# Kernel tuning notes

Measured on AMD Instinct MI355X. Metric: run time of the kernel, lower is better.

The kernel has to match this reference:

```python
import jax, jax.numpy as jnp
import numpy as np
from functools import partial

ALPHA = 0.5
BETA = 0.5
THRESHOLD = 0.5


def _ccl(fg):
    """Connected-component labeling (4-connectivity) of a 2D bool mask via
    iterative min-label propagation; background = 0, components get distinct
    positive ids (component-wise min of raster index + 1). Matches the
    component partition of scipy.ndimage.label (ids differ, masks identical)."""
    H, W = fg.shape
    BIG = H * W + 2
    init = jnp.where(fg, jnp.arange(1, H * W + 1, dtype=jnp.int32).reshape(H, W), 0)

    def step(lab):
        l = jnp.where(fg, lab, BIG)
        up = jnp.pad(l, ((1, 0), (0, 0)), constant_values=BIG)[:-1]
        dn = jnp.pad(l, ((0, 1), (0, 0)), constant_values=BIG)[1:]
        lf = jnp.pad(l, ((0, 0), (1, 0)), constant_values=BIG)[:, :-1]
        rt = jnp.pad(l, ((0, 0), (0, 1)), constant_values=BIG)[:, 1:]
        m = jnp.minimum(jnp.minimum(jnp.minimum(up, dn), jnp.minimum(lf, rt)), l)
        return jnp.where(fg, m, 0)

    def cond(c):
        return jnp.any(c[0] != c[1])

    def body(c):
        return (step(c[0]), c[0])

    lab, _ = jax.lax.while_loop(cond, body, (step(init), init))
    return lab


def _critical(a_lab, b_lab, n_seg):
    """Binary mask of components of a_lab that are not fully covered by the
    foreground of b_lab (i.e. contain at least one mistake voxel) -- the
    detect_critical split/merge criterion."""
    miss = ((b_lab == 0) & (a_lab > 0)).astype(jnp.int32)
    counts = jax.ops.segment_sum(miss.ravel(), a_lab.ravel(), num_segments=n_seg)
    return jnp.where(a_lab > 0, (counts[a_lab] > 0).astype(jnp.float32), 0.0)


def _critical_masks(preds, targets):
    # preds/targets: [B,1,H,W]; work on channel-0 2D slices as the module does
    p2 = preds[:, 0]
    t2 = targets[:, 0]
    H, W = p2.shape[-2:]
    n_seg = H * W + 1
    plab = jax.vmap(_ccl)(p2 > THRESHOLD)
    tlab = jax.vmap(_ccl)(t2 > 0)
    crit = jax.vmap(partial(_critical, n_seg=n_seg))
    neg = crit(tlab, plab)   # critical_type = -1: target components missed
    pos = crit(plab, tlab)   # critical_type = +1: pred components wrong
    return BETA * neg + (1.0 - BETA) * pos  # [B,H,W]


def setup_inputs() -> dict:
    key = jax.random.key(0)
    k1, k2 = jax.random.split(key)
    preds = jax.random.normal(k1, (16, 1, 1024, 1024), dtype=jnp.float32)
    targets = (jax.random.uniform(k2, (16, 1, 1024, 1024)) > 0.5).astype(jnp.float32)
    return {"preds": preds, "targets": targets}


def reference(preds, targets):
    # BCEWithLogitsLoss(reduction='none'), numerically stable
    loss = jnp.maximum(preds, 0) - preds * targets + jnp.log1p(jnp.exp(-jnp.abs(preds)))
    mask = _critical_masks(preds, targets)  # [B,H,W], constant wrt grads
    weight = (1.0 - ALPHA) + ALPHA * mask[:, None]  # broadcast over channel dim
    return (weight * loss).mean()
```

## Files before the change

kernel.cpp:

```cpp
#include <hip/hip_runtime.h>
#include <math.h>


#define HH 1024
#define WW 1024
#define IMGPIX (HH * WW)
#define NB_TOTAL 16
#define FLAGBIT 0x40000000
#define IDXMASK 0x3FFFFFFF
#define NBLK 2048
#define NPART 2048
#define NTHR 256
#define WPR 16
#define RPR 512
#define SROWS 32
#define STRIPS (HH / SROWS)
#define SLOTS (SROWS * RPR)
#define NTHR_S 1024

typedef unsigned long long u64;

__device__ __forceinline__ int findRootH(int* p, int i) {
    volatile int* vp = p;
    int r = i;
    int e = vp[r] & IDXMASK;
    while (e != r) {
        int e2 = vp[e] & IDXMASK;
        if (e2 != e) p[r] = e2;
        r = e; e = e2;
    }
    return r;
}

__device__ __forceinline__ void flagProp(int* p, int x) {
    while (true) {
        int r = findRootH(p, x);
        int old = atomicOr(&p[r], FLAGBIT);
        if ((old & IDXMASK) == r) return;
        x = old & IDXMASK;
    }
}

__device__ __forceinline__ void uniteGF(int* p, int a, int b) {
    int ra = findRootH(p, a), rb = findRootH(p, b);
    while (ra != rb) {
        if (ra < rb) { int t = ra; ra = rb; rb = t; }
        int e = p[ra];
        if ((e & IDXMASK) != ra) { ra = findRootH(p, e & IDXMASK); continue; }
        int prev = atomicCAS(&p[ra], e, rb);
        if (prev == e) {
            if (e & FLAGBIT) flagProp(p, rb);
            return;
        }
        ra = findRootH(p, prev & IDXMASK);
        rb = findRootH(p, rb);
    }
}

__device__ __forceinline__ int findRootL(int* lab, int i) {
    volatile int* vl = lab;
    int r = i;
    int e = vl[r] & IDXMASK;
    while (e != r) {
        int e2 = vl[e] & IDXMASK;
        if (e2 != e) lab[r] = e2;
        r = e; e = e2;
    }
    return r;
}

__device__ __forceinline__ void uniteL(int* lab, int a, int b) {
    int ra = findRootL(lab, a), rb = findRootL(lab, b);
    while (ra != rb) {
        if (ra < rb) { int t = ra; ra = rb; rb = t; }
        int prev = atomicCAS(&lab[ra], ra, rb);
        if (prev == ra) return;
        ra = findRootL(lab, prev & IDXMASK);
        rb = findRootL(lab, rb);
    }
}

__device__ __forceinline__ int runIndexW(u64 starts, int b) {
    u64 below = (2ULL << b) - 1ULL;
    return (int)__popcll(starts & below) - 1;
}

__global__ void k_zero(double* __restrict__ part) {
    part[blockIdx.x * blockDim.x + threadIdx.x] = 0.0;
}

__global__ void k_maskloss(const float* __restrict__ preds, const float* __restrict__ targets,
                           long gbase, int nrows,
                           u64* __restrict__ fT, u64* __restrict__ fP,
                           u64* __restrict__ sT, u64* __restrict__ sP,
                           int* __restrict__ prT, int* __restrict__ prP,
                           int* __restrict__ rcT, int* __restrict__ rcP,
                           _Float16* __restrict__ lossH, double* __restrict__ part) {
    int wid = threadIdx.x >> 6, lane = threadIdx.x & 63;
    double lsum = 0.0;
    for (int R = blockIdx.x * 4 + wid; R < nrows; R += gridDim.x * 4) {
        long pixbase = (long)R * WW;
        u64 myW = 0;
        #pragma unroll 4
        for (int w = 0; w < WPR; ++w) {
            long g = gbase + pixbase + w * 64 + lane;
            float p = preds[g], t = targets[g];
            float loss = fmaxf(p, 0.0f) - p * t + __logf(1.0f + __expf(-fabsf(p)));
            lossH[pixbase + w * 64 + lane] = (_Float16)loss;
            lsum += (double)loss;
            u64 bt = __ballot(t > 0.0f);
            u64 bp = __ballot(p > 0.5f);
            if (lane == w) myW = bt;
            if (lane == w + 16) myW = bp;
        }
        if (lane < 32) {
            int subid = lane & 15;
            u64 prevW = __shfl_up(myW, 1, 16);
            u64 carry = (subid > 0) ? (prevW >> 63) : 0ULL;
            u64 st = myW & ~((myW << 1) | carry);
            int cnt = (int)__popcll(st);
            int incl = cnt;
            #pragma unroll
            for (int d = 1; d < 16; d <<= 1) {
                int v = __shfl_up(incl, d, 16);
                if (subid >= d) incl += v;
            }
            int excl = incl - cnt;
            int wi = R * WPR + subid;
            if (lane < 16) {
                fT[wi] = myW; sT[wi] = st; prT[wi] = excl;
                if (subid == 15) rcT[R] = incl;
            } else {
                fP[wi] = myW; sP[wi] = st; prP[wi] = excl;
                if (subid == 15) rcP[R] = incl;
            }
        }
    }
    lsum *= 0.5;
    #pragma unroll
    for (int off = 32; off > 0; off >>= 1) lsum += __shfl_down(lsum, off, 64);
    __shared__ double sh[4];
    if (lane == 0) sh[wid] = lsum;
    __syncthreads();
    if (threadIdx.x == 0) part[blockIdx.x] += sh[0] + sh[1] + sh[2] + sh[3];
}

__global__ __launch_bounds__(NTHR_S) void
k_strip(const u64* __restrict__ fT, const u64* __restrict__ fP,
        const u64* __restrict__ sT, const u64* __restrict__ sP,
        const int* __restrict__ prT, const int* __restrict__ prP,
        const int* __restrict__ rcT, const int* __restrict__ rcP,
        int* __restrict__ parentT, int* __restrict__ parentP) {
    __shared__ int lab[SLOTS];
    __shared__ int rcL[SROWS];
    int bid = blockIdx.x;
    int ph = bid & 1; bid >>= 1;
    int strip = bid & (STRIPS - 1);
    int img = bid >> 5;
    const u64* f = ph ? fP : fT;
    const u64* fB = ph ? fT : fP;
    const u64* s = ph ? sP : sT;
    const int* pr = ph ? prP : prT;
    const int* rc = ph ? rcP : rcT;
    int* parent = ph ? parentP : parentT;
    const int row0 = img * HH + strip * SROWS;

    if (threadIdx.x < SROWS) rcL[threadIdx.x] = rc[row0 + threadIdx.x];
    __syncthreads();

    for (int i = threadIdx.x; i < SLOTS; i += NTHR_S)
        if ((i & (RPR - 1)) < rcL[i >> 9]) lab[i] = i;
    __syncthreads();

    for (int task = threadIdx.x; task < (SROWS - 1) * WPR * 2; task += NTHR_S) {
        int j = task & 1, w = (task >> 1) & 15, r = task >> 5;
        int w0 = (row0 + r) * WPR + w, w1 = w0 + WPR;
        u64 o = f[w0] & f[w1];
        if (!o) continue;
        u64 s0 = s[w0], s1 = s[w1];
        int b0 = r * RPR + pr[w0], b1 = (r + 1) * RPR + pr[w1];
        u64 os = o & ~(o << 1);
        int k = 0;
        while (os) {
            int b = __builtin_ctzll(os);
            os &= os - 1;
            if ((k++ & 1) == j)
                uniteL(lab, b0 + runIndexW(s0, b), b1 + runIndexW(s1, b));
        }
    }
    __syncthreads();

    for (int task = threadIdx.x; task < SROWS * WPR * 2; task += NTHR_S) {
        int j = task & 1, w = (task >> 1) & 15, r = task >> 5;
        int wi = (row0 + r) * WPR + w;
        u64 m = f[wi] & ~fB[wi];
        if (!m) continue;
        u64 sw = s[wi];
        int base = r * RPR + pr[wi];
        u64 ms = m & ~(m << 1);
        int k = 0, last = -1;
        while (ms) {
            int b = __builtin_ctzll(ms);
            ms &= ms - 1;
            if ((k++ & 1) != j) continue;
            int rid = base + runIndexW(sw, b);
            if (rid == last) continue;
            last = rid;
            int rt = findRootL(lab, rid);
            if (!(((volatile int*)lab)[rt] & FLAGBIT)) atomicOr(&lab[rt], FLAGBIT);
        }
    }
    __syncthreads();

    const int gb = row0 * RPR;
    for (int i = threadIdx.x; i < SLOTS; i += NTHR_S) {
        if ((i & (RPR - 1)) >= rcL[i >> 9]) continue;
        int e = lab[i];
        int rt = e & IDXMASK;
        if (rt != i) rt = findRootL(lab, rt);
        parent[gb + i] = (rt == i) ? ((gb + i) | (e & FLAGBIT)) : (gb + rt);
    }
}

__global__ void k_bound(const u64* __restrict__ fT, const u64* __restrict__ fP,
                        const u64* __restrict__ sT, const u64* __restrict__ sP,
                        const int* __restrict__ prT, const int* __restrict__ prP,
                        int* __restrict__ parentT, int* __restrict__ parentP, int nb) {
    int tasks = nb * (STRIPS - 1) * WPR * 2;
    int stride = gridDim.x * blockDim.x;
    for (int id = blockIdx.x * blockDim.x + threadIdx.x; id < tasks; id += stride) {
        int ph = id & 1;
        int t = id >> 1;
        int w = t & 15; t >>= 4;
        int bnd = t % (STRIPS - 1);
        int img = t / (STRIPS - 1);
        int R = img * HH + bnd * SROWS + (SROWS - 1);
        const u64* f = ph ? fP : fT;
        const u64* s = ph ? sP : sT;
        const int* pr = ph ? prP : prT;
        int* parent = ph ? parentP : parentT;
        int w0 = R * WPR + w, w1 = w0 + WPR;
        u64 o = f[w0] & f[w1];
        if (!o) continue;
        u64 s0 = s[w0], s1 = s[w1];
        int b0 = R * RPR + pr[w0], b1 = (R + 1) * RPR + pr[w1];
        u64 os = o & ~(o << 1);
        while (os) {
            int b = __builtin_ctzll(os);
            os &= os - 1;
            uniteGF(parent, b0 + runIndexW(s0, b), b1 + runIndexW(s1, b));
        }
    }
}

__global__ void k_flagfold(const int* __restrict__ rcT, const int* __restrict__ rcP,
                           int* __restrict__ parentT, int* __restrict__ parentP,
                           u64* __restrict__ flagT, u64* __restrict__ flagP, int nfw) {
    int stride = gridDim.x * blockDim.x;
    for (int id = blockIdx.x * blockDim.x + threadIdx.x; id < 2 * nfw; id += stride) {
        int ph = id >= nfw;
        int fw = ph ? id - nfw : id;
        int row = fw >> 3, k = fw & 7;
        const int* rc = ph ? rcP : rcT;
        int* parent = ph ? parentP : parentT;
        u64* flags = ph ? flagP : flagT;
        int cnt = rc[row];
        int s0 = k * 64;
        int s1 = min(s0 + 64, cnt);
        u64 bits = 0;
        int base = row * RPR;
        for (int sidx = s0; sidx < s1; ++sidx) {
            int i = base + sidx;
            int e = parent[i];
            int r = e & IDXMASK;
            int fl;
            if (r == i) fl = e & FLAGBIT;
            else { r = findRootH(parent, r); fl = parent[r] & FLAGBIT; }
            if (fl) bits |= 1ULL << (sidx - s0);
        }
        flags[fw] = bits;
    }
}

__global__ void k_accumflag(const _Float16* __restrict__ lossH, int npx4,
                            const u64* __restrict__ fT, const u64* __restrict__ fP,
                            const u64* __restrict__ sT, const u64* __restrict__ sP,
                            const int* __restrict__ prT, const int* __restrict__ prP,
                            const u64* __restrict__ flagT, const u64* __restrict__ flagP,
                            double* __restrict__ part) {
    int stride = gridDim.x * blockDim.x;
    double local = 0.0;
    const ushort4* lh4 = (const ushort4*)lossH;
    for (int i = blockIdx.x * blockDim.x + threadIdx.x; i < npx4; i += stride) {
        int px = i << 2;
        int R = px >> 10;
        int wi = R * WPR + ((px >> 6) & 15);
        u64 ft = fT[wi], fp = fP[wi];
        int b0 = px & 63;
        u64 mask4 = 0xFULL << b0;
        bool anyT = (ft & mask4) != 0, anyP = (fp & mask4) != 0;
        if (!anyT && !anyP) continue;
        ushort4 lw = lh4[i];
        u64 st = 0, sq = 0;
        int baseT = 0, baseP = 0;
        if (anyT) { st = sT[wi]; baseT = R * RPR + prT[wi]; }
        if (anyP) { sq = sP[wi]; baseP = R * RPR + prP[wi]; }
        unsigned short la[4] = {lw.x, lw.y, lw.z, lw.w};
        int lastT = -1, lastP = -1;
        float flagTv = 0.0f, flagPv = 0.0f;
        #pragma unroll
        for (int jj = 0; jj < 4; ++jj) {
            int b = b0 + jj;
            bool ftb = (ft >> b) & 1, fpb = (fp >> b) & 1;
            if (!(ftb || fpb)) continue;
            union { unsigned short u; _Float16 h; } cv;
            cv.u = la[jj];
            float loss = (float)cv.h;
            float c = 0.0f;
            if (ftb) {
                int rid = baseT + runIndexW(st, b);
                if (rid != lastT) {
                    lastT = rid;
                    flagTv = ((flagT[rid >> 6] >> (rid & 63)) & 1) ? 0.25f : 0.0f;
                }
                c += flagTv;
            }
            if (fpb) {
                int rid = baseP + runIndexW(sq, b);
                if (rid != lastP) {
                    lastP = rid;
                    flagPv = ((flagP[rid >> 6] >> (rid & 63)) & 1) ? 0.25f : 0.0f;
                }
                c += flagPv;
            }
            local += (double)(c * loss);
        }
    }
    #pragma unroll
    for (int off = 32; off > 0; off >>= 1) local += __shfl_down(local, off, 64);
    __shared__ double sh[NTHR / 64];
    int lane = threadIdx.x & 63, wid = threadIdx.x >> 6;
    if (lane == 0) sh[wid] = local;
    __syncthreads();
    if (threadIdx.x == 0) {
        double tot = 0.0;
        #pragma unroll
        for (int w = 0; w < NTHR / 64; ++w) tot += sh[w];
        part[blockIdx.x] += tot;
    }
}

__global__ void k_final(const double* __restrict__ part, float* __restrict__ out, double inv_n) {
    double v = 0.0;
    for (int i = threadIdx.x; i < NPART; i += blockDim.x) v += part[i];
    #pragma unroll
    for (int off = 32; off > 0; off >>= 1) v += __shfl_down(v, off, 64);
    __shared__ double sh[NTHR / 64];
    int lane = threadIdx.x & 63, wid = threadIdx.x >> 6;
    if (lane == 0) sh[wid] = v;
    __syncthreads();
    if (threadIdx.x == 0) {
        double tot = 0.0;
        #pragma unroll
        for (int w = 0; w < NTHR / 64; ++w) tot += sh[w];
        out[0] = (float)(tot * inv_n);
    }
}

extern "C" void kernel_launch(void* const* d_in, const int* in_sizes, int n_in,
                              void* d_out, int out_size, void* d_ws, size_t ws_size,
                              hipStream_t stream) {
    const float* preds = (const float*)d_in[0];
    const float* targets = (const float*)d_in[1];
    float* out = (float*)d_out;

    double* part = (double*)d_ws;
    char* base = (char*)d_ws + NPART * sizeof(double);
    size_t avail = (ws_size > NPART * sizeof(double)) ? ws_size - NPART * sizeof(double) : 0;
    const size_t wpi = (size_t)HH * WPR;
    const size_t runs_pi = (size_t)HH * RPR;
    const size_t fw_pi = runs_pi / 64;
    const size_t per_img = 4 * wpi * sizeof(u64) + 2 * wpi * sizeof(int)
                         + 2 * HH * sizeof(int) + 2 * runs_pi * sizeof(int)
                         + 2 * fw_pi * sizeof(u64) + (size_t)IMGPIX * 2;
    int chunk = (int)(avail / per_img);
    if (chunk < 1) chunk = 1;
    if (chunk > NB_TOTAL) chunk = NB_TOTAL;

    u64* fT = (u64*)base;
    u64* fP = fT + (size_t)chunk * wpi;
    u64* sT = fP + (size_t)chunk * wpi;
    u64* sP = sT + (size_t)chunk * wpi;
    int* prT = (int*)(sP + (size_t)chunk * wpi);
    int* prP = prT + (size_t)chunk * wpi;
    int* rcT = prP + (size_t)chunk * wpi;
    int* rcP = rcT + (size_t)chunk * HH;
    int* parentT = rcP + (size_t)chunk * HH;
    int* parentP = parentT + (size_t)chunk * runs_pi;
    u64* flagT = (u64*)(parentP + (size_t)chunk * runs_pi);
    u64* flagP = flagT + (size_t)chunk * fw_pi;
    _Float16* lossH = (_Float16*)(flagP + (size_t)chunk * fw_pi);

    k_zero<<<NPART / NTHR, NTHR, 0, stream>>>(part);

    for (int b0 = 0; b0 < NB_TOTAL; b0 += chunk) {
        int nb = (b0 + chunk <= NB_TOTAL) ? chunk : (NB_TOTAL - b0);
        int npx = nb * IMGPIX;
        long gbase = (long)b0 * IMGPIX;
        int nrows = nb * HH;
        int nfw = (int)(nb * fw_pi);

        k_maskloss<<<NBLK, NTHR, 0, stream>>>(preds, targets, gbase, nrows,
                                              fT, fP, sT, sP, prT, prP, rcT, rcP,
                                              lossH, part);
        k_strip<<<nb * STRIPS * 2, NTHR_S, 0, stream>>>(fT, fP, sT, sP, prT, prP,
                                                        rcT, rcP, parentT, parentP);
        k_bound<<<128, NTHR, 0, stream>>>(fT, fP, sT, sP, prT, prP, parentT, parentP, nb);
        k_flagfold<<<1024, NTHR, 0, stream>>>(rcT, rcP, parentT, parentP, flagT, flagP, nfw);
        k_accumflag<<<NBLK, NTHR, 0, stream>>>(lossH, npx >> 2, fT, fP, sT, sP,
                                               prT, prP, flagT, flagP, part);
    }

    double inv_n = 1.0 / ((double)NB_TOTAL * (double)IMGPIX);
    k_final<<<1, NTHR, 0, stream>>>(part, out, inv_n);
}
```

Before: 279.0 us.

## Pre-aggregate loss per run in maskloss and fuse flag lookup with accumulation

```diff
diff --git a/kernel.cpp b/kernel.cpp
--- a/kernel.cpp
+++ b/kernel.cpp
@@ -95,21 +95,36 @@
                            u64* __restrict__ sT, u64* __restrict__ sP,
                            int* __restrict__ prT, int* __restrict__ prP,
                            int* __restrict__ rcT, int* __restrict__ rcP,
-                           _Float16* __restrict__ lossH, double* __restrict__ part) {
+                           float* __restrict__ runsumT, float* __restrict__ runsumP,
+                           double* __restrict__ part) {
+    __shared__ float rsT[4][RPR];
+    __shared__ float rsP[4][RPR];
+    __shared__ double sh[4];
     int wid = threadIdx.x >> 6, lane = threadIdx.x & 63;
     double lsum = 0.0;
-    for (int R = blockIdx.x * 4 + wid; R < nrows; R += gridDim.x * 4) {
+    for (int rbase = blockIdx.x * 4; rbase < nrows; rbase += gridDim.x * 4) {
+        int R = rbase + wid;
         long pixbase = (long)R * WW;
+        for (int k = lane; k < RPR; k += 64) { rsT[wid][k] = 0.0f; rsP[wid][k] = 0.0f; }
+        __syncthreads();
         u64 myW = 0;
+        int cumT = 0, cumP = 0;
+        u64 carryT = 0, carryP = 0;
         #pragma unroll 4
         for (int w = 0; w < WPR; ++w) {
             long g = gbase + pixbase + w * 64 + lane;
             float p = preds[g], t = targets[g];
             float loss = fmaxf(p, 0.0f) - p * t + __logf(1.0f + __expf(-fabsf(p)));
-            lossH[pixbase + w * 64 + lane] = (_Float16)loss;
             lsum += (double)loss;
-            u64 bt = __ballot(t > 0.0f);
-            u64 bp = __ballot(p > 0.5f);
+            bool tf = t > 0.0f, pf = p > 0.5f;
+            u64 bt = __ballot(tf);
+            u64 bp = __ballot(pf);
+            u64 stT = bt & ~((bt << 1) | carryT);
+            u64 stP = bp & ~((bp << 1) | carryP);
+            if (tf) atomicAdd(&rsT[wid][cumT + runIndexW(stT, lane)], loss);
+            if (pf) atomicAdd(&rsP[wid][cumP + runIndexW(stP, lane)], loss);
+            cumT += (int)__popcll(stT); carryT = bt >> 63;
+            cumP += (int)__popcll(stP); carryP = bp >> 63;
             if (lane == w) myW = bt;
             if (lane == w + 16) myW = bp;
         }
@@ -135,11 +150,14 @@
                 if (subid == 15) rcP[R] = incl;
             }
         }
+        __syncthreads();
+        for (int k = lane; k < cumT; k += 64) runsumT[(long)R * RPR + k] = rsT[wid][k];
+        for (int k = lane; k < cumP; k += 64) runsumP[(long)R * RPR + k] = rsP[wid][k];
+        __syncthreads();
     }
     lsum *= 0.5;
     #pragma unroll
     for (int off = 32; off > 0; off >>= 1) lsum += __shfl_down(lsum, off, 64);
-    __shared__ double sh[4];
     if (lane == 0) sh[wid] = lsum;
     __syncthreads();
     if (threadIdx.x == 0) part[blockIdx.x] += sh[0] + sh[1] + sh[2] + sh[3];
@@ -253,87 +271,29 @@
     }
 }
 
-__global__ void k_flagfold(const int* __restrict__ rcT, const int* __restrict__ rcP,
+__global__ void k_accumrun(const int* __restrict__ rcT, const int* __restrict__ rcP,
                            int* __restrict__ parentT, int* __restrict__ parentP,
-                           u64* __restrict__ flagT, u64* __restrict__ flagP, int nfw) {
+                           const float* __restrict__ runsumT, const float* __restrict__ runsumP,
+                           double* __restrict__ part, int nslots) {
     int stride = gridDim.x * blockDim.x;
-    for (int id = blockIdx.x * blockDim.x + threadIdx.x; id < 2 * nfw; id += stride) {
-        int ph = id >= nfw;
-        int fw = ph ? id - nfw : id;
-        int row = fw >> 3, k = fw & 7;
-        const int* rc = ph ? rcP : rcT;
-        int* parent = ph ? parentP : parentT;
-        u64* flags = ph ? flagP : flagT;
-        int cnt = rc[row];
-        int s0 = k * 64;
-        int s1 = min(s0 + 64, cnt);
-        u64 bits = 0;
-        int base = row * RPR;
-        for (int sidx = s0; sidx < s1; ++sidx) {
-            int i = base + sidx;
-            int e = parent[i];
+    double local = 0.0;
+    for (int i = blockIdx.x * blockDim.x + threadIdx.x; i < nslots; i += stride) {
+        int row = i >> 9, k = i & (RPR - 1);
+        if (k < rcT[row]) {
+            int e = parentT[i];
             int r = e & IDXMASK;
             int fl;
             if (r == i) fl = e & FLAGBIT;
-            else { r = findRootH(parent, r); fl = parent[r] & FLAGBIT; }
-            if (fl) bits |= 1ULL << (sidx - s0);
-        }
-        flags[fw] = bits;
-    }
-}
-
-__global__ void k_accumflag(const _Float16* __restrict__ lossH, int npx4,
-                            const u64* __restrict__ fT, const u64* __restrict__ fP,
-                            const u64* __restrict__ sT, const u64* __restrict__ sP,
-                            const int* __restrict__ prT, const int* __restrict__ prP,
-                            const u64* __restrict__ flagT, const u64* __restrict__ flagP,
-                            double* __restrict__ part) {
-    int stride = gridDim.x * blockDim.x;
-    double local = 0.0;
-    const ushort4* lh4 = (const ushort4*)lossH;
-    for (int i = blockIdx.x * blockDim.x + threadIdx.x; i < npx4; i += stride) {
-        int px = i << 2;
-        int R = px >> 10;
-        int wi = R * WPR + ((px >> 6) & 15);
-        u64 ft = fT[wi], fp = fP[wi];
-        int b0 = px & 63;
-        u64 mask4 = 0xFULL << b0;
-        bool anyT = (ft & mask4) != 0, anyP = (fp & mask4) != 0;
-        if (!anyT && !anyP) continue;
-        ushort4 lw = lh4[i];
-        u64 st = 0, sq = 0;
-        int baseT = 0, baseP = 0;
-        if (anyT) { st = sT[wi]; baseT = R * RPR + prT[wi]; }
-        if (anyP) { sq = sP[wi]; baseP = R * RPR + prP[wi]; }
-        unsigned short la[4] = {lw.x, lw.y, lw.z, lw.w};
-        int lastT = -1, lastP = -1;
-        float flagTv = 0.0f, flagPv = 0.0f;
-        #pragma unroll
-        for (int jj = 0; jj < 4; ++jj) {
-            int b = b0 + jj;
-            bool ftb = (ft >> b) & 1, fpb = (fp >> b) & 1;
-            if (!(ftb || fpb)) continue;
-            union { unsigned short u; _Float16 h; } cv;
-            cv.u = la[jj];
-            float loss = (float)cv.h;
-            float c = 0.0f;
-            if (ftb) {
-                int rid = baseT + runIndexW(st, b);
-                if (rid != lastT) {
-                    lastT = rid;
-                    flagTv = ((flagT[rid >> 6] >> (rid & 63)) & 1) ? 0.25f : 0.0f;
-                }
-                c += flagTv;
-            }
-            if (fpb) {
-                int rid = baseP + runIndexW(sq, b);
-                if (rid != lastP) {
-                    lastP = rid;
-                    flagPv = ((flagP[rid >> 6] >> (rid & 63)) & 1) ? 0.25f : 0.0f;
-                }
-                c += flagPv;
-            }
-            local += (double)(c * loss);
+            else { r = findRootH(parentT, r); fl = parentT[r] & FLAGBIT; }
+            if (fl) local += 0.25 * (double)runsumT[i];
+        }
+        if (k < rcP[row]) {
+            int e = parentP[i];
+            int r = e & IDXMASK;
+            int fl;
+            if (r == i) fl = e & FLAGBIT;
+            else { r = findRootH(parentP, r); fl = parentP[r] & FLAGBIT; }
+            if (fl) local += 0.25 * (double)runsumP[i];
         }
     }
     #pragma unroll
@@ -379,10 +339,9 @@
     size_t avail = (ws_size > NPART * sizeof(double)) ? ws_size - NPART * sizeof(double) : 0;
     const size_t wpi = (size_t)HH * WPR;
     const size_t runs_pi = (size_t)HH * RPR;
-    const size_t fw_pi = runs_pi / 64;
     const size_t per_img = 4 * wpi * sizeof(u64) + 2 * wpi * sizeof(int)
                          + 2 * HH * sizeof(int) + 2 * runs_pi * sizeof(int)
-                         + 2 * fw_pi * sizeof(u64) + (size_t)IMGPIX * 2;
+                         + 2 * runs_pi * sizeof(float);
     int chunk = (int)(avail / per_img);
     if (chunk < 1) chunk = 1;
     if (chunk > NB_TOTAL) chunk = NB_TOTAL;
@@ -397,28 +356,25 @@
     int* rcP = rcT + (size_t)chunk * HH;
     int* parentT = rcP + (size_t)chunk * HH;
     int* parentP = parentT + (size_t)chunk * runs_pi;
-    u64* flagT = (u64*)(parentP + (size_t)chunk * runs_pi);
-    u64* flagP = flagT + (size_t)chunk * fw_pi;
-    _Float16* lossH = (_Float16*)(flagP + (size_t)chunk * fw_pi);
+    float* runsumT = (float*)(parentP + (size_t)chunk * runs_pi);
+    float* runsumP = runsumT + (size_t)chunk * runs_pi;
 
     k_zero<<<NPART / NTHR, NTHR, 0, stream>>>(part);
 
     for (int b0 = 0; b0 < NB_TOTAL; b0 += chunk) {
         int nb = (b0 + chunk <= NB_TOTAL) ? chunk : (NB_TOTAL - b0);
-        int npx = nb * IMGPIX;
         long gbase = (long)b0 * IMGPIX;
         int nrows = nb * HH;
-        int nfw = (int)(nb * fw_pi);
+        int nslots = (int)(nb * runs_pi);
 
         k_maskloss<<<NBLK, NTHR, 0, stream>>>(preds, targets, gbase, nrows,
                                               fT, fP, sT, sP, prT, prP, rcT, rcP,
-                                              lossH, part);
+                                              runsumT, runsumP, part);
         k_strip<<<nb * STRIPS * 2, NTHR_S, 0, stream>>>(fT, fP, sT, sP, prT, prP,
                                                         rcT, rcP, parentT, parentP);
         k_bound<<<128, NTHR, 0, stream>>>(fT, fP, sT, sP, prT, prP, parentT, parentP, nb);
-        k_flagfold<<<1024, NTHR, 0, stream>>>(rcT, rcP, parentT, parentP, flagT, flagP, nfw);
-        k_accumflag<<<NBLK, NTHR, 0, stream>>>(lossH, npx >> 2, fT, fP, sT, sP,
-                                               prT, prP, flagT, flagP, part);
+        k_accumrun<<<NBLK, NTHR, 0, stream>>>(rcT, rcP, parentT, parentP,
+                                              runsumT, runsumP, part, nslots);
     }
 
     double inv_n = 1.0 / ((double)NB_TOTAL * (double)IMGPIX);
```

Result: slower. 306.7 us (+9.9%).
